# Performance work log

Hardware: AMD Instinct MI355X
Metric: run time of the kernel (lower is better)

The kernel has to match this reference:

```python
import jax, jax.numpy as jnp
import numpy as np

HIDDEN = 1024
B, S = 64, 512
EPS = 1e-10


def setup_inputs() -> dict:
    key = jax.random.key(0)
    k1, k2, k3, k4, k5 = jax.random.split(key, 5)
    encoder_outputs = jax.random.normal(k1, (B, S, HIDDEN), dtype=jnp.float32)
    decoder_hidden = jax.random.normal(k2, (B, HIDDEN), dtype=jnp.float32)
    inp_mask = (jax.random.uniform(k3, (S, B)) > 0.2).astype(jnp.float32)
    # W_h: Linear(2H -> H, bias=False); torch stores weight as (out, in)
    W_h = jax.random.normal(k4, (HIDDEN, 2 * HIDDEN), dtype=jnp.float32) / np.sqrt(2 * HIDDEN)
    stdv = 1.0 / np.sqrt(HIDDEN)
    v = jax.random.normal(k5, (HIDDEN,), dtype=jnp.float32) * stdv
    return {"encoder_outputs": encoder_outputs, "decoder_hidden": decoder_hidden,
            "inp_mask": inp_mask, "W_h": W_h, "v": v}


def reference(encoder_outputs, decoder_hidden, inp_mask, W_h, v):
    # encoder_outputs: [B, S, H]; decoder_hidden: [B, H]; inp_mask: [S, B]
    seq_len = encoder_outputs.shape[1]
    # H = decoder_hidden broadcast over seq: [B, S, H] (avoid explicit repeat)
    Hrep = jnp.broadcast_to(decoder_hidden[:, None, :], encoder_outputs.shape)
    cat = jnp.concatenate([Hrep, encoder_outputs], axis=2)          # [B, S, 2H]
    energy = jnp.tanh(jnp.einsum('bsk,hk->bsh', cat, W_h))          # [B, S, H]
    scores = jnp.einsum('bsh,h->bs', energy, v)                     # [B, S]
    # NOTE: original applies softmax over dim=0 (the batch dim) — faithful here
    a = jax.nn.softmax(scores, axis=0) * inp_mask.T                 # [B, S]
    a = a / (jnp.sum(a, axis=1, keepdims=True) + EPS)
    context = jnp.einsum('bs,bsh->bh', a, encoder_outputs)[:, None, :]  # [B, 1, H]
    return a[:, None, :], context
```

## Files before the change

### kernel.cpp

```cpp
#include <hip/hip_runtime.h>

#define B_ 64
#define S_ 512
#define H_ 1024
#define M_ (B_*S_)

typedef unsigned int u32;
typedef unsigned short u16;
typedef __attribute__((ext_vector_type(8))) short bf16x8;
typedef __attribute__((ext_vector_type(4))) float f32x4;

__device__ __forceinline__ u16 f2bf(float f) {
  u32 u = __builtin_bit_cast(u32, f);
  u += 0x7fffu + ((u >> 16) & 1u);
  return (u16)(u >> 16);
}
__device__ __forceinline__ u32 pk2(float a, float b) {
  return (u32)f2bf(a) | ((u32)f2bf(b) << 16);
}
__device__ __forceinline__ float tanh_fast(float x) {
  x = fminf(fmaxf(x, -20.f), 20.f);
  float e = __expf(2.f * x);
  return (e - 1.f) / (e + 1.f);
}
__device__ __forceinline__ void gload_lds16(const u16* g, u16* l) {
  __builtin_amdgcn_global_load_lds(
      (const __attribute__((address_space(1))) u32*)g,
      (__attribute__((address_space(3))) u32*)l, 16, 0, 0);
}

__device__ __forceinline__ void decode_bid(int bid, int& r0, int& n0) {
  int nt = (bid >> 3) & 7;
  int rp = ((bid >> 6) << 3) | (bid & 7);
  r0 = rp * 128; n0 = nt * 128;
}

__global__ void conv_enc(const float* __restrict__ e, u16* __restrict__ o) {
  int g0 = blockIdx.x * 2048 + threadIdx.x;
#pragma unroll
  for (int j = 0; j < 8; ++j) {
    int g = g0 + j * 256;
    const float4* s = (const float4*)(e + (size_t)g * 8);
    float4 x = s[0], y = s[1];
    uint4 p;
    p.x = pk2(x.x, x.y); p.y = pk2(x.z, x.w);
    p.z = pk2(y.x, y.y); p.w = pk2(y.z, y.w);
    *(uint4*)(o + (size_t)g * 8) = p;
  }
}

__global__ void conv_w2(const float* __restrict__ Wh, u16* __restrict__ W2bf) {
  int idx = blockIdx.x * 256 + threadIdx.x;
  int n = idx >> 8;
  int k = (idx & 255) * 4;
  float4 x = *(const float4*)(Wh + (size_t)n * 2048 + 1024 + k);
  uint2 p; p.x = pk2(x.x, x.y); p.y = pk2(x.z, x.w);
  *(uint2*)(W2bf + (size_t)n * 1024 + k) = p;
}

__global__ void part1_kernel(const float* __restrict__ dh,
                             const float* __restrict__ Wh,
                             float* __restrict__ part1) {
  __shared__ float whs[16][132];
  __shared__ float dhs[64][132];
  int t = threadIdx.x;
  int h0 = blockIdx.x * 16;
  int b = t >> 2, hg = t & 3;
  float acc[4] = {0.f, 0.f, 0.f, 0.f};
  for (int kc = 0; kc < 8; ++kc) {
    int k0 = kc * 128;
    __syncthreads();
#pragma unroll
    for (int i = 0; i < 2; ++i) {
      int idx = t + 256 * i; int r = idx >> 5, c4 = idx & 31;
      *(float4*)&whs[r][c4 * 4] =
          *(const float4*)(Wh + (size_t)(h0 + r) * 2048 + k0 + c4 * 4);
    }
#pragma unroll
    for (int i = 0; i < 8; ++i) {
      int idx = t + 256 * i; int r = idx >> 5, c4 = idx & 31;
      *(float4*)&dhs[r][c4 * 4] =
          *(const float4*)(dh + (size_t)r * 1024 + k0 + c4 * 4);
    }
    __syncthreads();
#pragma unroll 4
    for (int k = 0; k < 128; ++k) {
      float d = dhs[b][k];
#pragma unroll
      for (int j = 0; j < 4; ++j) acc[j] += whs[hg * 4 + j][k] * d;
    }
  }
#pragma unroll
  for (int j = 0; j < 4; ++j) part1[b * 1024 + h0 + hg * 4 + j] = acc[j];
}

__global__ __launch_bounds__(256, 2) void gemm_scores_bf(
    const u16* __restrict__ Abf, const u16* __restrict__ W2bf,
    const float* __restrict__ part1, const float* __restrict__ v,
    float* __restrict__ scores_part) {
  __shared__ __align__(16) u16 As[2][128 * 64];
  __shared__ __align__(16) u16 Bs[2][128 * 64];
  __shared__ float sc_lds[128];
  const int tid = threadIdx.x;
  const int lane = tid & 63, wid = tid >> 6;
  const int wr = wid >> 1, wc = wid & 1;
  const int l15 = lane & 15, lhi = lane >> 4;
  int r0, n0; decode_bid(blockIdx.x, r0, n0);
  const int nt = n0 >> 7;
  const int bb = r0 >> 9;
  f32x4 acc[4][4] = {};

  int sofs[4];
#pragma unroll
  for (int i = 0; i < 4; ++i) {
    int idx = i * 256 + tid;
    int row = idx >> 3, g = idx & 7;
    sofs[i] = row * 1024 + ((g ^ (row & 7)) << 3);
  }

#define STAGE_T(pbuf, kk0)                                                   \
  do {                                                                       \
    _Pragma("unroll") for (int i_ = 0; i_ < 4; ++i_)                         \
        gload_lds16(Abf + (size_t)r0 * 1024 + (kk0) + sofs[i_],              \
                    &As[pbuf][i_ * 2048 + wid * 512]);                       \
    _Pragma("unroll") for (int i_ = 0; i_ < 4; ++i_)                         \
        gload_lds16(W2bf + (size_t)n0 * 1024 + (kk0) + sofs[i_],             \
                    &Bs[pbuf][i_ * 2048 + wid * 512]);                       \
  } while (0)

  STAGE_T(0, 0);
  __syncthreads();
  int p = 0;
  for (int t = 0; t < 16; ++t) {
    if (t < 15) STAGE_T(p ^ 1, (t + 1) * 64);
#pragma unroll
    for (int kk = 0; kk < 2; ++kk) {
      bf16x8 af[4], bfr[4];
#pragma unroll
      for (int i = 0; i < 4; ++i) {
        int ar = wr * 64 + i * 16 + l15;
        af[i] = *(const bf16x8*)
            &As[p][ar * 64 + (((kk * 4 + lhi) ^ (ar & 7)) << 3)];
      }
#pragma unroll
      for (int j = 0; j < 4; ++j) {
        int br = wc * 64 + j * 16 + l15;
        bfr[j] = *(const bf16x8*)
            &Bs[p][br * 64 + (((kk * 4 + lhi) ^ (br & 7)) << 3)];
      }
#pragma unroll
      for (int i = 0; i < 4; ++i)
#pragma unroll
        for (int j = 0; j < 4; ++j)
          acc[i][j] = __builtin_amdgcn_mfma_f32_16x16x32_bf16(
              af[i], bfr[j], acc[i][j], 0, 0, 0);
    }
    __syncthreads();
    p ^= 1;
  }
#undef STAGE_T

  if (tid < 128) sc_lds[tid] = 0.f;
  __syncthreads();
  float ps[4][4] = {};
#pragma unroll
  for (int j = 0; j < 4; ++j) {
    int col = n0 + wc * 64 + j * 16 + l15;
    float pv = part1[bb * 1024 + col];
    float vv = v[col];
#pragma unroll
    for (int i = 0; i < 4; ++i)
#pragma unroll
      for (int q = 0; q < 4; ++q)
        ps[i][q] += tanh_fast(acc[i][j][q] + pv) * vv;
  }
#pragma unroll
  for (int i = 0; i < 4; ++i)
#pragma unroll
    for (int q = 0; q < 4; ++q)
      atomicAdd(&sc_lds[wr * 64 + i * 16 + lhi * 4 + q], ps[i][q]);
  __syncthreads();
  if (tid < 128) scores_part[nt * M_ + r0 + tid] = sc_lds[tid];
}

__global__ __launch_bounds__(256, 2) void gemm_scores_inline(
    const float* __restrict__ enc, const u16* __restrict__ W2bf,
    const float* __restrict__ part1, const float* __restrict__ v,
    float* __restrict__ scores_part) {
  __shared__ __align__(16) u16 As[2][128 * 64];
  __shared__ __align__(16) u16 Bs[2][128 * 64];
  __shared__ float sc_lds[128];
  const int tid = threadIdx.x;
  const int lane = tid & 63, wid = tid >> 6;
  const int wr = wid >> 1, wc = wid & 1;
  const int l15 = lane & 15, lhi = lane >> 4;
  int r0, n0; decode_bid(blockIdx.x, r0, n0);
  const int nt = n0 >> 7;
  const int bb = r0 >> 9;
  f32x4 acc[4][4] = {};
  const int brow8 = lane >> 3;
  const int bks = ((lane & 7) ^ brow8) * 8;
  {
#pragma unroll
    for (int c = 0; c < 4; ++c)
      gload_lds16(W2bf + (size_t)(n0 + c * 32 + wid * 8 + brow8) * 1024 + bks,
                  &Bs[0][c * 2048 + wid * 512]);
#pragma unroll
    for (int i = 0; i < 4; ++i) {
      int f = 2 * tid + 512 * i;
      int arow = f >> 4, c4 = f & 15;
      const float4* srcA =
          (const float4*)(enc + (size_t)(r0 + arow) * 1024 + c4 * 4);
      float4 x = srcA[0], y = srcA[1];
      uint4 pw; pw.x = pk2(x.x, x.y); pw.y = pk2(x.z, x.w);
      pw.z = pk2(y.x, y.y); pw.w = pk2(y.z, y.w);
      *(uint4*)&As[0][arow * 64 + ((c4 * 4) ^ ((arow & 7) << 3))] = pw;
    }
    __syncthreads();
  }
  int p = 0;
  for (int t = 0; t < 16; ++t) {
    float4 xa[4], ya[4];
    if (t < 15) {
      const int kn = (t + 1) * 64;
#pragma unroll
      for (int c = 0; c < 4; ++c)
        gload_lds16(
            W2bf + (size_t)(n0 + c * 32 + wid * 8 + brow8) * 1024 + kn + bks,
            &Bs[p ^ 1][c * 2048 + wid * 512]);
#pragma unroll
      for (int i = 0; i < 4; ++i) {
        int f = 2 * tid + 512 * i;
        int arow = f >> 4, c4 = f & 15;
        const float4* srcA =
            (const float4*)(enc + (size_t)(r0 + arow) * 1024 + kn + c4 * 4);
        xa[i] = srcA[0]; ya[i] = srcA[1];
      }
    }
#pragma unroll
    for (int kk = 0; kk < 2; ++kk) {
      bf16x8 af[4], bfr[4];
#pragma unroll
      for (int i = 0; i < 4; ++i) {
        int ar = wr * 64 + i * 16 + l15;
        af[i] = *(const bf16x8*)
            &As[p][ar * 64 + ((kk * 32 + lhi * 8) ^ ((ar & 7) << 3))];
      }
#pragma unroll
      for (int j = 0; j < 4; ++j) {
        int br = wc * 64 + j * 16 + l15;
        bfr[j] = *(const bf16x8*)
            &Bs[p][br * 64 + ((kk * 32 + lhi * 8) ^ ((br & 7) << 3))];
      }
#pragma unroll
      for (int i = 0; i < 4; ++i)
#pragma unroll
        for (int j = 0; j < 4; ++j)
          acc[i][j] = __builtin_amdgcn_mfma_f32_16x16x32_bf16(
              af[i], bfr[j], acc[i][j], 0, 0, 0);
    }
    if (t < 15) {
#pragma unroll
      for (int i = 0; i < 4; ++i) {
        int f = 2 * tid + 512 * i;
        int arow = f >> 4, c4 = f & 15;
        uint4 pw;
        pw.x = pk2(xa[i].x, xa[i].y); pw.y = pk2(xa[i].z, xa[i].w);
        pw.z = pk2(ya[i].x, ya[i].y); pw.w = pk2(ya[i].z, ya[i].w);
        *(uint4*)&As[p ^ 1][arow * 64 + ((c4 * 4) ^ ((arow & 7) << 3))] = pw;
      }
      __syncthreads();
      p ^= 1;
    }
  }
  if (tid < 128) sc_lds[tid] = 0.f;
  __syncthreads();
  float ps[4][4] = {};
#pragma unroll
  for (int j = 0; j < 4; ++j) {
    int col = n0 + wc * 64 + j * 16 + l15;
    float pv = part1[bb * 1024 + col];
    float vv = v[col];
#pragma unroll
    for (int i = 0; i < 4; ++i)
#pragma unroll
      for (int q = 0; q < 4; ++q)
        ps[i][q] += tanh_fast(acc[i][j][q] + pv) * vv;
  }
#pragma unroll
  for (int i = 0; i < 4; ++i)
#pragma unroll
    for (int q = 0; q < 4; ++q)
      atomicAdd(&sc_lds[wr * 64 + i * 16 + lhi * 4 + q], ps[i][q]);
  __syncthreads();
  if (tid < 128) scores_part[nt * M_ + r0 + tid] = sc_lds[tid];
}

__global__ void softmax_col(const float* __restrict__ sp,
                            const float* __restrict__ mask,
                            float* __restrict__ a_raw) {
  int s = blockIdx.x * 4 + (threadIdx.x >> 6);
  int b = threadIdx.x & 63;
  float x = 0.f;
#pragma unroll
  for (int n = 0; n < 8; ++n) x += sp[n * M_ + b * 512 + s];
  float m = x;
  for (int o = 32; o; o >>= 1) m = fmaxf(m, __shfl_xor(m, o));
  float e = __expf(x - m);
  float sum = e;
  for (int o = 32; o; o >>= 1) sum += __shfl_xor(sum, o);
  a_raw[b * 512 + s] = (e / sum) * mask[s * 64 + b];
}

__global__ void norm_rows(const float* __restrict__ a_raw,
                          float* __restrict__ out_a) {
  __shared__ float wsum[4];
  int b = blockIdx.x, t = threadIdx.x;
  float va = a_raw[b * 512 + t];
  float vb = a_raw[b * 512 + 256 + t];
  float sum = va + vb;
  for (int o = 32; o; o >>= 1) sum += __shfl_xor(sum, o);
  if ((t & 63) == 0) wsum[t >> 6] = sum;
  __syncthreads();
  float tot = wsum[0] + wsum[1] + wsum[2] + wsum[3];
  float inv = 1.f / (tot + 1e-10f);
  out_a[b * 512 + t] = va * inv;
  out_a[b * 512 + 256 + t] = vb * inv;
}

__global__ void context_kernel(const float* __restrict__ a,
                               const float* __restrict__ enc,
                               float* __restrict__ ctx) {
  __shared__ float red[128];
  int b = blockIdx.x, hc = blockIdx.y, t = threadIdx.x;
  int h = hc * 128 + (t & 127);
  int sh = t >> 7;
  const float* ep = enc + (size_t)b * 524288 + (size_t)sh * 262144 + h;
  const float* ap = a + b * 512 + sh * 256;
  float acc = 0.f;
#pragma unroll 8
  for (int s = 0; s < 256; ++s) acc += ap[s] * ep[(size_t)s * 1024];
  if (sh) red[t & 127] = acc;
  __syncthreads();
  if (!sh) ctx[b * 1024 + h] = acc + red[t];
}

extern "C" void kernel_launch(void* const* d_in, const int* in_sizes, int n_in,
                              void* d_out, int out_size, void* d_ws,
                              size_t ws_size, hipStream_t stream) {
  const float* enc  = (const float*)d_in[0];
  const float* dh   = (const float*)d_in[1];
  const float* mask = (const float*)d_in[2];
  const float* Wh   = (const float*)d_in[3];
  const float* v    = (const float*)d_in[4];
  float* out_a   = (float*)d_out;
  float* out_ctx = out_a + M_;

  char* ws = (char*)d_ws;
  const size_t SZ_ENC = (size_t)M_ * H_ * 2;
  u16*   W2bf; u16* encbf = nullptr;
  float *part1, *sp, *a_raw;
  bool big = ws_size >= SZ_ENC + (4u << 20);
  if (big) {
    encbf = (u16*)ws;
    W2bf  = (u16*)(ws + SZ_ENC);
    part1 = (float*)(ws + SZ_ENC + (2u << 20));
    sp    = (float*)(ws + SZ_ENC + (2u << 20) + (256u << 10));
    a_raw = (float*)(ws + SZ_ENC + (2u << 20) + (256u << 10) + (1u << 20));
  } else {
    W2bf  = (u16*)ws;
    part1 = (float*)(ws + (2u << 20));
    sp    = (float*)(ws + (2u << 20) + (256u << 10));
    a_raw = (float*)(ws + (2u << 20) + (256u << 10) + (1u << 20));
  }

  conv_w2<<<1024, 256, 0, stream>>>(Wh, W2bf);
  part1_kernel<<<64, 256, 0, stream>>>(dh, Wh, part1);
  if (big) {
    conv_enc<<<2048, 256, 0, stream>>>(enc, encbf);
    gemm_scores_bf<<<2048, 256, 0, stream>>>(encbf, W2bf, part1, v, sp);
  } else {
    gemm_scores_inline<<<2048, 256, 0, stream>>>(enc, W2bf, part1, v, sp);
  }
  softmax_col<<<128, 256, 0, stream>>>(sp, mask, a_raw);
  norm_rows<<<64, 256, 0, stream>>>(a_raw, out_a);
  context_kernel<<<dim3(64, 8), 256, 0, stream>>>(out_a, enc, out_ctx);
}
```

Baseline: 436.0 us.

## Deepen GEMM prefetch, transpose score layout, fuse row sums, split context reduction

The bf16 GEMM now keeps two stages in flight. It uses explicit vmcnt waits, raw barriers and setprio in place of full syncthreads, so global-to-LDS loads overlap the MFMA work. Partial scores are written transposed so the softmax over batch reads coalesced data, and the softmax kernel also accumulates per-row sums atomically, which removes the separate norm pass. The context stage is split over sequence chunks with float4 loads and a final reduce kernel, and part1 uses vectorised LDS reads. In exchange there are more launches, a memset, and a larger workspace threshold for the big path, which could drop to the inline path if the workspace is small.

Result: faster. 415.1 us (-4.8%).

```diff
diff --git a/kernel.cpp b/kernel.cpp
--- a/kernel.cpp
+++ b/kernel.cpp
@@ -84,10 +84,13 @@
     }
     __syncthreads();
 #pragma unroll 4
-    for (int k = 0; k < 128; ++k) {
-      float d = dhs[b][k];
-#pragma unroll
-      for (int j = 0; j < 4; ++j) acc[j] += whs[hg * 4 + j][k] * d;
+    for (int k4 = 0; k4 < 32; ++k4) {
+      float4 d = *(const float4*)&dhs[b][k4 * 4];
+#pragma unroll
+      for (int j = 0; j < 4; ++j) {
+        float4 w = *(const float4*)&whs[hg * 4 + j][k4 * 4];
+        acc[j] += w.x * d.x + w.y * d.y + w.z * d.z + w.w * d.w;
+      }
     }
   }
 #pragma unroll
@@ -97,7 +100,7 @@
 __global__ __launch_bounds__(256, 2) void gemm_scores_bf(
     const u16* __restrict__ Abf, const u16* __restrict__ W2bf,
     const float* __restrict__ part1, const float* __restrict__ v,
-    float* __restrict__ scores_part) {
+    float* __restrict__ spT) {
   __shared__ __align__(16) u16 As[2][128 * 64];
   __shared__ __align__(16) u16 Bs[2][128 * 64];
   __shared__ float sc_lds[128];
@@ -129,10 +132,15 @@
   } while (0)
 
   STAGE_T(0, 0);
-  __syncthreads();
-  int p = 0;
+  STAGE_T(1, 64);
+
   for (int t = 0; t < 16; ++t) {
-    if (t < 15) STAGE_T(p ^ 1, (t + 1) * 64);
+    const int p = t & 1;
+    if (t < 15) asm volatile("s_waitcnt vmcnt(8)" ::: "memory");
+    else        asm volatile("s_waitcnt vmcnt(0)" ::: "memory");
+    __builtin_amdgcn_s_barrier();
+    __builtin_amdgcn_sched_barrier(0);
+    __builtin_amdgcn_s_setprio(1);
 #pragma unroll
     for (int kk = 0; kk < 2; ++kk) {
       bf16x8 af[4], bfr[4];
@@ -155,8 +163,10 @@
           acc[i][j] = __builtin_amdgcn_mfma_f32_16x16x32_bf16(
               af[i], bfr[j], acc[i][j], 0, 0, 0);
     }
-    __syncthreads();
-    p ^= 1;
+    __builtin_amdgcn_s_setprio(0);
+    __builtin_amdgcn_sched_barrier(0);
+    __builtin_amdgcn_s_barrier();
+    if (t < 14) STAGE_T(p, (t + 2) * 64);
   }
 #undef STAGE_T
 
@@ -180,13 +190,16 @@
     for (int q = 0; q < 4; ++q)
       atomicAdd(&sc_lds[wr * 64 + i * 16 + lhi * 4 + q], ps[i][q]);
   __syncthreads();
-  if (tid < 128) scores_part[nt * M_ + r0 + tid] = sc_lds[tid];
+  if (tid < 128) {
+    int row = r0 + tid;
+    spT[nt * M_ + (row & 511) * 64 + (row >> 9)] = sc_lds[tid];
+  }
 }
 
 __global__ __launch_bounds__(256, 2) void gemm_scores_inline(
     const float* __restrict__ enc, const u16* __restrict__ W2bf,
     const float* __restrict__ part1, const float* __restrict__ v,
-    float* __restrict__ scores_part) {
+    float* __restrict__ spT) {
   __shared__ __align__(16) u16 As[2][128 * 64];
   __shared__ __align__(16) u16 Bs[2][128 * 64];
   __shared__ float sc_lds[128];
@@ -293,56 +306,69 @@
     for (int q = 0; q < 4; ++q)
       atomicAdd(&sc_lds[wr * 64 + i * 16 + lhi * 4 + q], ps[i][q]);
   __syncthreads();
-  if (tid < 128) scores_part[nt * M_ + r0 + tid] = sc_lds[tid];
-}
-
-__global__ void softmax_col(const float* __restrict__ sp,
-                            const float* __restrict__ mask,
-                            float* __restrict__ a_raw) {
-  int s = blockIdx.x * 4 + (threadIdx.x >> 6);
-  int b = threadIdx.x & 63;
+  if (tid < 128) {
+    int row = r0 + tid;
+    spT[nt * M_ + (row & 511) * 64 + (row >> 9)] = sc_lds[tid];
+  }
+}
+
+__global__ void softmax_colT(const float* __restrict__ spT,
+                             const float* __restrict__ mask,
+                             float* __restrict__ a_rawT,
+                             float* __restrict__ rowsum) {
+  __shared__ float red[4][64];
+  int t = threadIdx.x;
+  int sl = t >> 6, b = t & 63;
+  int s = blockIdx.x * 4 + sl;
   float x = 0.f;
 #pragma unroll
-  for (int n = 0; n < 8; ++n) x += sp[n * M_ + b * 512 + s];
+  for (int n = 0; n < 8; ++n) x += spT[n * M_ + s * 64 + b];
   float m = x;
   for (int o = 32; o; o >>= 1) m = fmaxf(m, __shfl_xor(m, o));
   float e = __expf(x - m);
   float sum = e;
   for (int o = 32; o; o >>= 1) sum += __shfl_xor(sum, o);
-  a_raw[b * 512 + s] = (e / sum) * mask[s * 64 + b];
-}
-
-__global__ void norm_rows(const float* __restrict__ a_raw,
-                          float* __restrict__ out_a) {
-  __shared__ float wsum[4];
-  int b = blockIdx.x, t = threadIdx.x;
-  float va = a_raw[b * 512 + t];
-  float vb = a_raw[b * 512 + 256 + t];
-  float sum = va + vb;
-  for (int o = 32; o; o >>= 1) sum += __shfl_xor(sum, o);
-  if ((t & 63) == 0) wsum[t >> 6] = sum;
+  float av = (e / sum) * mask[s * 64 + b];
+  a_rawT[s * 64 + b] = av;
+  red[sl][b] = av;
   __syncthreads();
-  float tot = wsum[0] + wsum[1] + wsum[2] + wsum[3];
-  float inv = 1.f / (tot + 1e-10f);
-  out_a[b * 512 + t] = va * inv;
-  out_a[b * 512 + 256 + t] = vb * inv;
-}
-
-__global__ void context_kernel(const float* __restrict__ a,
-                               const float* __restrict__ enc,
-                               float* __restrict__ ctx) {
-  __shared__ float red[128];
-  int b = blockIdx.x, hc = blockIdx.y, t = threadIdx.x;
-  int h = hc * 128 + (t & 127);
-  int sh = t >> 7;
-  const float* ep = enc + (size_t)b * 524288 + (size_t)sh * 262144 + h;
-  const float* ap = a + b * 512 + sh * 256;
-  float acc = 0.f;
+  if (sl == 0)
+    atomicAdd(&rowsum[b], red[0][b] + red[1][b] + red[2][b] + red[3][b]);
+}
+
+__global__ void write_a(const float* __restrict__ a_rawT,
+                        const float* __restrict__ rowsum,
+                        float* __restrict__ out_a) {
+  int b = blockIdx.x, s = threadIdx.x;
+  float inv = 1.f / (rowsum[b] + 1e-10f);
+  out_a[b * 512 + s] = a_rawT[s * 64 + b] * inv;
+}
+
+__global__ void context_part(const float* __restrict__ a_rawT,
+                             const float* __restrict__ rowsum,
+                             const float* __restrict__ enc,
+                             float* __restrict__ ctx_part) {
+  int b = blockIdx.x, sc = blockIdx.y, t = threadIdx.x;
+  float inv = 1.f / (rowsum[b] + 1e-10f);
+  const float* ep = enc + (size_t)b * 524288 + (size_t)sc * 65536;
+  f32x4 acc = {0.f, 0.f, 0.f, 0.f};
 #pragma unroll 8
-  for (int s = 0; s < 256; ++s) acc += ap[s] * ep[(size_t)s * 1024];
-  if (sh) red[t & 127] = acc;
-  __syncthreads();
-  if (!sh) ctx[b * 1024 + h] = acc + red[t];
+  for (int s = 0; s < 64; ++s) {
+    float av = a_rawT[(sc * 64 + s) * 64 + b] * inv;
+    float4 e = *(const float4*)(ep + (size_t)s * 1024 + t * 4);
+    acc.x += av * e.x; acc.y += av * e.y;
+    acc.z += av * e.z; acc.w += av * e.w;
+  }
+  *(f32x4*)(ctx_part + ((size_t)sc * 64 + b) * 1024 + t * 4) = acc;
+}
+
+__global__ void reduce_ctx(const float* __restrict__ ctx_part,
+                           float* __restrict__ out_ctx) {
+  int idx = blockIdx.x * 256 + threadIdx.x;
+  float s = 0.f;
+#pragma unroll
+  for (int c = 0; c < 8; ++c) s += ctx_part[(size_t)c * 65536 + idx];
+  out_ctx[idx] = s;
 }
 
 extern "C" void kernel_launch(void* const* d_in, const int* in_sizes, int n_in,
@@ -358,31 +384,29 @@
 
   char* ws = (char*)d_ws;
   const size_t SZ_ENC = (size_t)M_ * H_ * 2;
-  u16*   W2bf; u16* encbf = nullptr;
-  float *part1, *sp, *a_raw;
-  bool big = ws_size >= SZ_ENC + (4u << 20);
-  if (big) {
-    encbf = (u16*)ws;
-    W2bf  = (u16*)(ws + SZ_ENC);
-    part1 = (float*)(ws + SZ_ENC + (2u << 20));
-    sp    = (float*)(ws + SZ_ENC + (2u << 20) + (256u << 10));
-    a_raw = (float*)(ws + SZ_ENC + (2u << 20) + (256u << 10) + (1u << 20));
-  } else {
-    W2bf  = (u16*)ws;
-    part1 = (float*)(ws + (2u << 20));
-    sp    = (float*)(ws + (2u << 20) + (256u << 10));
-    a_raw = (float*)(ws + (2u << 20) + (256u << 10) + (1u << 20));
-  }
-
+  u16* W2bf; u16* encbf = nullptr;
+  char* base;
+  bool big = ws_size >= SZ_ENC + (8u << 20);
+  if (big) { encbf = (u16*)ws; base = ws + SZ_ENC; }
+  else     { base = ws; }
+  W2bf            = (u16*)base;
+  float* part1    = (float*)(base + (2u << 20));
+  float* spT      = (float*)(base + (2u << 20) + (256u << 10));
+  float* a_rawT   = (float*)(base + (3u << 20) + (256u << 10));
+  float* rowsum   = (float*)(base + (3u << 20) + (384u << 10));
+  float* ctx_part = (float*)(base + (3u << 20) + (512u << 10));
+
+  hipMemsetAsync(rowsum, 0, 64 * sizeof(float), stream);
   conv_w2<<<1024, 256, 0, stream>>>(Wh, W2bf);
   part1_kernel<<<64, 256, 0, stream>>>(dh, Wh, part1);
   if (big) {
     conv_enc<<<2048, 256, 0, stream>>>(enc, encbf);
-    gemm_scores_bf<<<2048, 256, 0, stream>>>(encbf, W2bf, part1, v, sp);
+    gemm_scores_bf<<<2048, 256, 0, stream>>>(encbf, W2bf, part1, v, spT);
   } else {
-    gemm_scores_inline<<<2048, 256, 0, stream>>>(enc, W2bf, part1, v, sp);
-  }
-  softmax_col<<<128, 256, 0, stream>>>(sp, mask, a_raw);
-  norm_rows<<<64, 256, 0, stream>>>(a_raw, out_a);
-  context_kernel<<<dim3(64, 8), 256, 0, stream>>>(out_a, enc, out_ctx);
-}
+    gemm_scores_inline<<<2048, 256, 0, stream>>>(enc, W2bf, part1, v, spT);
+  }
+  softmax_colT<<<128, 256, 0, stream>>>(spT, mask, a_rawT, rowsum);
+  write_a<<<64, 512, 0, stream>>>(a_rawT, rowsum, out_a);
+  context_part<<<dim3(64, 8), 256, 0, stream>>>(a_rawT, rowsum, enc, ctx_part);
+  reduce_ctx<<<256, 256, 0, stream>>>(ctx_part, out_ctx);
+}
```
